# Optimization experiments

Hardware: AMD Instinct MI355X
Metric: run time of the kernel (lower is better)

The kernel has to match this reference:

```python
import jax, jax.numpy as jnp
import numpy as np

COST_CLASS, COST_BBOX, COST_MASK = 1.0, 5.0, 2.0
EPS = 1e-6


def setup_inputs() -> dict:
    key = jax.random.key(0)
    k = jax.random.split(key, 8)
    B, Q, M, C1, H, W = 8, 300, 100, 81, 128, 128
    pred_logits = jax.random.normal(k[0], (B, Q, C1), jnp.float32)
    # boxes as valid xyxy in [0,1]: lo in [0,.5], size in [0,.5]
    plo = jax.random.uniform(k[1], (B, Q, 2)) * 0.5
    psz = jax.random.uniform(k[2], (B, Q, 2)) * 0.5
    pred_boxes = jnp.concatenate([plo, plo + psz], axis=-1)
    pred_masks = jax.random.normal(k[3], (B, Q, H, W), jnp.float32)
    gt_labels = jax.random.randint(k[4], (B, M), 0, C1, dtype=jnp.int32)
    glo = jax.random.uniform(k[5], (B, M, 2)) * 0.5
    gsz = jax.random.uniform(k[6], (B, M, 2)) * 0.5
    gt_boxes = jnp.concatenate([glo, glo + gsz], axis=-1)
    gt_masks = (jax.random.uniform(k[7], (B, M, H, W)) > 0.5).astype(jnp.float32)
    valid = jnp.ones((B, M), jnp.bool_)
    return dict(pred_logits=pred_logits, pred_boxes=pred_boxes, pred_masks=pred_masks,
                gt_labels=gt_labels, gt_boxes=gt_boxes, gt_masks=gt_masks, valid=valid)


def _giou(b1, b2):
    # b1 [Q,4], b2 [M,4] (xyxy) -> [Q,M] generalized IoU
    lt = jnp.maximum(b1[:, None, :2], b2[None, :, :2])
    rb = jnp.minimum(b1[:, None, 2:], b2[None, :, 2:])
    wh = jnp.clip(rb - lt, 0.0)
    inter = wh[..., 0] * wh[..., 1]
    a1 = (b1[:, 2] - b1[:, 0]) * (b1[:, 3] - b1[:, 1])
    a2 = (b2[:, 2] - b2[:, 0]) * (b2[:, 3] - b2[:, 1])
    union = a1[:, None] + a2[None, :] - inter
    iou = inter / (union + EPS)
    ltm = jnp.minimum(b1[:, None, :2], b2[None, :, :2])
    rbm = jnp.maximum(b1[:, None, 2:], b2[None, :, 2:])
    whm = jnp.clip(rbm - ltm, 0.0)
    am = whm[..., 0] * whm[..., 1]
    return iou - (am - union) / (am + EPS)


@jax.jit
def _cost_matrix(pred_logits, pred_boxes, pred_masks, gt_labels, gt_boxes, gt_masks):
    B, Q = pred_logits.shape[:2]
    M = gt_labels.shape[1]
    probs = jax.nn.softmax(pred_logits, axis=-1)                      # [B,Q,C+1]
    idx = jnp.broadcast_to(gt_labels[:, None, :].astype(jnp.int32), (B, Q, M))
    cost_class = -jnp.take_along_axis(probs, idx, axis=2)             # [B,Q,M]
    # L1 cdist
    cost_bbox = jnp.abs(pred_boxes[:, :, None, :] - gt_boxes[:, None, :, :]).sum(-1)
    cost_giou = -jax.vmap(_giou)(pred_boxes, gt_boxes)                # [B,Q,M]
    # dice cost
    pm = jax.nn.sigmoid(pred_masks).reshape(B, Q, -1)                 # [B,Q,HW]
    gm = gt_masks.reshape(B, M, -1).astype(pm.dtype)                  # [B,M,HW]
    num = 2.0 * jnp.einsum('bqc,bmc->bqm', pm, gm)
    den = pm.sum(-1)[:, :, None] + gm.sum(-1)[:, None, :]
    cost_mask = 1.0 - num / (den + EPS)
    # NOTE: faithful to source quirk -- giou term is folded into cost_bbox
    # and therefore weighted by COST_BBOX.
    return (COST_CLASS * cost_class + COST_BBOX * (cost_bbox + cost_giou)
            + COST_MASK * cost_mask)


def _hungarian(cost):
    # Jonker-Volgenant style shortest-augmenting-path assignment (e-maxx).
    # cost: np [n,m] with n <= m. Returns p[m]: row assigned to each col (-1 if none).
    n, m = cost.shape
    u = np.zeros(n)
    v = np.zeros(m)
    p = np.full(m, -1, np.int64)
    for i in range(n):
        minv = np.full(m, np.inf)
        way = np.full(m, -1, np.int64)
        used = np.zeros(m, bool)
        cur_row, j0 = i, -1
        while True:
            cur = cost[cur_row] - u[cur_row] - v
            upd = (~used) & (cur < minv)
            minv[upd] = cur[upd]
            way[upd] = j0
            mv = np.where(used, np.inf, minv)
            j1 = int(np.argmin(mv))
            delta = mv[j1]
            u[i] += delta
            uj = np.nonzero(used)[0]
            if uj.size:
                u[p[uj]] += delta
                v[uj] -= delta
            minv[~used] -= delta
            used[j1] = True
            j0 = j1
            cur_row = p[j1]
            if cur_row == -1:
                break
        j = j0
        while j != -1:
            jp = way[j]
            p[j] = p[jp] if jp != -1 else i
            j = jp
    return p


def reference(pred_logits, pred_boxes, pred_masks, gt_labels, gt_boxes, gt_masks, valid):
    # valid is all-ones (num_gt == max_objects for every sample), so the
    # per-sample variable-size slicing in the torch loop reduces to full M.
    C = _cost_matrix(pred_logits, pred_boxes, pred_masks, gt_labels, gt_boxes, gt_masks)
    Cn = np.asarray(C, dtype=np.float64)
    preds, gts = [], []
    for b in range(Cn.shape[0]):
        # solve on transpose: rows = gt (M=100) <= cols = queries (Q=300)
        p = _hungarian(Cn[b].T)            # p[q] = matched gt index or -1
        q = np.nonzero(p >= 0)[0]          # sorted pred indices (scipy convention)
        preds.append(q)
        gts.append(p[q])
    pred_idx = jnp.asarray(np.stack(preds), dtype=jnp.int32)  # [B, M]
    gt_idx = jnp.asarray(np.stack(gts), dtype=jnp.int32)      # [B, M]
    return C, pred_idx, gt_idx
```

## Files before the change

kernel.cpp:

```cpp
#include <hip/hip_runtime.h>

#define HW 16384
#define NQ 300
#define NM 100
#define NB 8
#define NC 81
#define KCH 1024
#define NKC 16
#define CTP 304

typedef __attribute__((ext_vector_type(8))) short frag8;
typedef __attribute__((ext_vector_type(4))) float float4v;
typedef __attribute__((ext_vector_type(4))) unsigned short ushort4v;

__device__ __forceinline__ unsigned short f2bf(float f) {
  union { float f; unsigned u; } c; c.f = f;
  unsigned r = c.u + 0x7FFFu + ((c.u >> 16) & 1u);
  return (unsigned short)(r >> 16);
}

__global__ __launch_bounds__(256) void prep_kernel(
    const float* __restrict__ pmask, const float* __restrict__ gmask,
    unsigned short* __restrict__ pm, unsigned short* __restrict__ gm,
    float* __restrict__ psum, float* __restrict__ gsum) {
  int row = blockIdx.x;
  int t = threadIdx.x;
  bool isP = row < NB * NQ;
  const float* srcf = isP ? (pmask + (size_t)row * HW)
                          : (gmask + (size_t)(row - NB * NQ) * HW);
  unsigned short* dst = isP ? (pm + (size_t)row * HW)
                            : (gm + (size_t)(row - NB * NQ) * HW);
  const float4v* src = (const float4v*)srcf;
  float s = 0.f;
  for (int i = t; i < HW / 4; i += 256) {
    float4v x = src[i];
    float y0, y1, y2, y3;
    if (isP) {
      y0 = 1.f / (1.f + __expf(-x.x));
      y1 = 1.f / (1.f + __expf(-x.y));
      y2 = 1.f / (1.f + __expf(-x.z));
      y3 = 1.f / (1.f + __expf(-x.w));
    } else { y0 = x.x; y1 = x.y; y2 = x.z; y3 = x.w; }
    s += (y0 + y1) + (y2 + y3);
    ushort4v o = { f2bf(y0), f2bf(y1), f2bf(y2), f2bf(y3) };
    *(ushort4v*)(dst + i * 4) = o;
  }
  for (int off = 32; off > 0; off >>= 1) s += __shfl_xor(s, off, 64);
  __shared__ float red[4];
  int wave = t >> 6, lane = t & 63;
  if (lane == 0) red[wave] = s;
  __syncthreads();
  if (t == 0) {
    float tot = (red[0] + red[1]) + (red[2] + red[3]);
    if (isP) psum[row] = tot; else gsum[row - NB * NQ] = tot;
  }
}

__global__ __launch_bounds__(256) void softmax_kernel(
    const float* __restrict__ logits, float* __restrict__ probs) {
  int wave = threadIdx.x >> 6, lane = threadIdx.x & 63;
  int row = blockIdx.x * 4 + wave;
  const float* in = logits + (size_t)row * NC;
  float x0 = (lane < NC) ? in[lane] : -1e30f;
  float x1 = (lane + 64 < NC) ? in[lane + 64] : -1e30f;
  float mx = fmaxf(x0, x1);
  for (int off = 32; off > 0; off >>= 1) mx = fmaxf(mx, __shfl_xor(mx, off, 64));
  float e0 = (lane < NC) ? __expf(x0 - mx) : 0.f;
  float e1 = (lane + 64 < NC) ? __expf(x1 - mx) : 0.f;
  float s = e0 + e1;
  for (int off = 32; off > 0; off >>= 1) s += __shfl_xor(s, off, 64);
  float inv = 1.f / s;
  if (lane < NC) probs[(size_t)row * NC + lane] = e0 * inv;
  if (lane + 64 < NC) probs[(size_t)row * NC + lane + 64] = e1 * inv;
}

__global__ __launch_bounds__(64) void dot_kernel(
    const unsigned short* __restrict__ pm, const unsigned short* __restrict__ gm,
    float* __restrict__ dotv) {
  int qt = blockIdx.x;
  int b = blockIdx.y >> 4, kc = blockIdx.y & 15;
  int lane = threadIdx.x;
  int q0 = qt * 16;
  int row_a = q0 + (lane & 15);
  int ra = (row_a < NQ) ? row_a : NQ - 1;
  int koff = (lane >> 4) * 8;
  const unsigned short* pA = pm + ((size_t)b * NQ + ra) * HW + kc * KCH + koff;
  const unsigned short* pB0 = gm + (size_t)b * NM * HW + kc * KCH + koff;
  const unsigned short* pB[7];
#pragma unroll
  for (int mt = 0; mt < 7; ++mt) {
    int row_b = mt * 16 + (lane & 15);
    int rb = (row_b < NM) ? row_b : NM - 1;
    pB[mt] = pB0 + (size_t)rb * HW;
  }
  float4v acc[7];
#pragma unroll
  for (int mt = 0; mt < 7; ++mt) acc[mt] = (float4v){0.f, 0.f, 0.f, 0.f};
#pragma unroll 2
  for (int k = 0; k < KCH; k += 32) {
    frag8 a = *(const frag8*)(pA + k);
#pragma unroll
    for (int mt = 0; mt < 7; ++mt) {
      frag8 bb = *(const frag8*)(pB[mt] + k);
      acc[mt] = __builtin_amdgcn_mfma_f32_16x16x32_bf16(a, bb, acc[mt], 0, 0, 0);
    }
  }
#pragma unroll
  for (int mt = 0; mt < 7; ++mt) {
    int cm = mt * 16 + (lane & 15);
    if (cm < NM) {
#pragma unroll
      for (int r = 0; r < 4; ++r) {
        int cq = q0 + (lane >> 4) * 4 + r;
        if (cq < NQ)
          unsafeAtomicAdd(&dotv[((size_t)b * NQ + cq) * NM + cm], acc[mt][r]);
      }
    }
  }
}

__global__ __launch_bounds__(256) void combine_kernel(
    const float* __restrict__ dotv, const float* __restrict__ psum,
    const float* __restrict__ gsum, const float* __restrict__ probs,
    const int* __restrict__ labels, const float* __restrict__ pboxes,
    const float* __restrict__ gboxes, float* __restrict__ outC,
    float* __restrict__ ct) {
  int idx = blockIdx.x * 256 + threadIdx.x;
  if (idx >= NB * NQ * NM) return;
  int b = idx / (NQ * NM);
  int r = idx - b * (NQ * NM);
  int q = r / NM;
  int m = r - q * NM;
  float num = 2.f * dotv[idx];
  float den = psum[b * NQ + q] + gsum[b * NM + m];
  float cmask = 1.f - num / (den + 1e-6f);
  int lab = labels[b * NM + m];
  float cclass = -probs[((size_t)b * NQ + q) * NC + lab];
  const float* pb = pboxes + ((size_t)b * NQ + q) * 4;
  const float* gb = gboxes + ((size_t)b * NM + m) * 4;
  float p0 = pb[0], p1 = pb[1], p2 = pb[2], p3 = pb[3];
  float g0 = gb[0], g1 = gb[1], g2 = gb[2], g3 = gb[3];
  float cbbox = fabsf(p0 - g0) + fabsf(p1 - g1) + fabsf(p2 - g2) + fabsf(p3 - g3);
  float iw = fmaxf(fminf(p2, g2) - fmaxf(p0, g0), 0.f);
  float ih = fmaxf(fminf(p3, g3) - fmaxf(p1, g1), 0.f);
  float inter = iw * ih;
  float a1 = (p2 - p0) * (p3 - p1), a2 = (g2 - g0) * (g3 - g1);
  float uni = a1 + a2 - inter;
  float iou = inter / (uni + 1e-6f);
  float aw = fmaxf(fmaxf(p2, g2) - fminf(p0, g0), 0.f);
  float ah = fmaxf(fmaxf(p3, g3) - fminf(p1, g1), 0.f);
  float am = aw * ah;
  float giou = iou - (am - uni) / (am + 1e-6f);
  float C = cclass + 5.f * (cbbox - giou) + 2.f * cmask;
  outC[idx] = C;
  ct[((size_t)b * NM + m) * CTP + q] = C;
}

__device__ __forceinline__ float wave_fmin_bcast(float x) {
  int t;
  t = __builtin_amdgcn_update_dpp(__float_as_int(x), __float_as_int(x), 0x111, 0xf, 0xf, false);
  x = fminf(x, __int_as_float(t));
  t = __builtin_amdgcn_update_dpp(__float_as_int(x), __float_as_int(x), 0x112, 0xf, 0xf, false);
  x = fminf(x, __int_as_float(t));
  t = __builtin_amdgcn_update_dpp(__float_as_int(x), __float_as_int(x), 0x114, 0xf, 0xf, false);
  x = fminf(x, __int_as_float(t));
  t = __builtin_amdgcn_update_dpp(__float_as_int(x), __float_as_int(x), 0x118, 0xf, 0xf, false);
  x = fminf(x, __int_as_float(t));
  t = __builtin_amdgcn_update_dpp(__float_as_int(x), __float_as_int(x), 0x142, 0xf, 0xf, false);
  x = fminf(x, __int_as_float(t));
  t = __builtin_amdgcn_update_dpp(__float_as_int(x), __float_as_int(x), 0x143, 0xf, 0xf, false);
  x = fminf(x, __int_as_float(t));
  return __int_as_float(__builtin_amdgcn_readlane(__float_as_int(x), 63));
}

extern __shared__ char hsmem[];
__global__ __launch_bounds__(64) void hungarian_kernel(
    const float* __restrict__ ct, float* __restrict__ out) {
  float* cost   = (float*)hsmem;
  float* u      = (float*)(hsmem + 121600);
  int*   p      = (int*)(hsmem + 122000);
  int*   way    = (int*)(hsmem + 123280);
  int*   colOwn = (int*)(hsmem + 124560);
  int*   rowUsed= (int*)(hsmem + 125840);
  int*   queue  = (int*)(hsmem + 126240);
  int*   qmisc  = (int*)(hsmem + 127840);
  int*   flist  = colOwn;
  const int b = blockIdx.x;
  const int lane = threadIdx.x;
  const float INF = __builtin_inff();

  {
    const float4v* a4 = (const float4v*)(ct + (size_t)b * NM * CTP);
    float4v* c4 = (float4v*)cost;
    for (int i = lane; i < NM * CTP / 4; i += 64) c4[i] = a4[i];
  }
#pragma unroll
  for (int w = 0; w < 5; ++w) {
    p[lane + 64 * w] = -1;
    colOwn[lane + 64 * w] = 0x7fffffff;
  }
  if (lane == 0) { qmisc[0] = 0; qmisc[1] = 0; }
  float v[5];
#pragma unroll
  for (int w = 0; w < 5; ++w) v[w] = 0.f;
  __syncthreads();

  int rarg0 = 0, rarg1 = 0;
  {
    int i = lane;
    float mv = INF; int cj = 0;
    for (int j = 0; j < NQ; ++j) {
      float c = cost[i * CTP + j];
      if (c < mv) { mv = c; cj = j; }
    }
    u[i] = mv; rarg0 = cj;
  }
  if (lane < NM - 64) {
    int i = lane + 64;
    float mv = INF; int cj = 0;
    for (int j = 0; j < NQ; ++j) {
      float c = cost[i * CTP + j];
      if (c < mv) { mv = c; cj = j; }
    }
    u[i] = mv; rarg1 = cj;
  }
  atomicMin(&colOwn[rarg0], lane);
  if (lane < NM - 64) atomicMin(&colOwn[rarg1], lane + 64);
  __syncthreads();
  int free0 = 0, free1 = 0;
  {
    bool won = (colOwn[rarg0] == lane);
    if (won) p[rarg0] = lane;
    rowUsed[lane] = won ? 1 : 0;
    free0 = won ? 0 : 1;
  }
  if (lane < NM - 64) {
    bool won = (colOwn[rarg1] == lane + 64);
    if (won) p[rarg1] = lane + 64;
    rowUsed[lane + 64] = won ? 1 : 0;
    free1 = won ? 0 : 1;
  }
  {
    unsigned long long m0 = __ballot(free0 != 0);
    if (free0) queue[__popcll(m0 & ((1ull << lane) - 1ull))] = lane;
    int base = (int)__popcll(m0);
    unsigned long long m1 = __ballot(free1 != 0);
    if (free1) queue[base + (int)__popcll(m1 & ((1ull << lane) - 1ull))] = lane + 64;
    base += (int)__popcll(m1);
    if (lane == 0) qmisc[1] = base;
  }

  int pops = 0;
  while (true) {
    __syncthreads();
    int h = qmisc[0], t = qmisc[1];
    if (h >= t || pops >= 192) break;
    int i = queue[h];
    ++pops;
    if (lane == 0) qmisc[0] = h + 1;
    float tv[5];
    float m1 = INF, m2 = INF;
#pragma unroll
    for (int w = 0; w < 5; ++w) {
      int j = lane + 64 * w;
      float tt = (j < NQ) ? (cost[i * CTP + j] - v[w]) : INF;
      tv[w] = tt;
      if (tt < m1) { m2 = m1; m1 = tt; } else if (tt < m2) m2 = tt;
    }
    float m1g = wave_fmin_bcast(m1);
    int j1 = -1;
#pragma unroll
    for (int w = 0; w < 5; ++w) {
      unsigned long long mk = __ballot(tv[w] == m1g);
      if (j1 < 0 && mk) j1 = (int)__builtin_ctzll(mk) + 64 * w;
    }
    float c2c = INF;
#pragma unroll
    for (int w = 0; w < 5; ++w)
      if (lane + 64 * w != j1) c2c = fminf(c2c, tv[w]);
    float c2 = wave_fmin_bcast(c2c);
    float delta = (c2 > m1g) ? (c2 - m1g) : 0.f;
    int i1 = p[j1];
    if (i1 >= 0 && delta <= 0.f) {
      if (lane == 0) u[i] = c2;
      continue;
    }
#pragma unroll
    for (int w = 0; w < 5; ++w) if (lane + 64 * w == j1) v[w] -= delta;
    if (lane == 0) {
      u[i] = c2;
      p[j1] = i;
      rowUsed[i] = 1;
      if (i1 >= 0) { rowUsed[i1] = 0; queue[t] = i1; qmisc[1] = t + 1; }
    }
  }
  __syncthreads();

  int nfree;
  {
    int r0 = rowUsed[lane];
    int r1 = (lane < NM - 64) ? rowUsed[lane + 64] : 1;
    unsigned long long m0 = __ballot(r0 == 0);
    if (!r0) flist[__popcll(m0 & ((1ull << lane) - 1ull))] = lane;
    int base = (int)__popcll(m0);
    unsigned long long m1 = __ballot(r1 == 0);
    if (!r1) flist[base + (int)__popcll(m1 & ((1ull << lane) - 1ull))] = lane + 64;
    nfree = base + (int)__popcll(m1);
  }
  __syncthreads();

  int pr0, pr1, pr2, pr3, pr4;
  float ur0, ur1;
  pr0 = p[lane]; pr1 = p[lane + 64]; pr2 = p[lane + 128];
  pr3 = p[lane + 192]; pr4 = p[lane + 256];
  ur0 = u[lane];
  ur1 = (lane < NM - 64) ? u[lane + 64] : 0.f;

  for (int fi = 0; fi < nfree; ++fi) {
    int i = flist[fi];
    float dv[5]; int usedR[5];
#pragma unroll
    for (int w = 0; w < 5; ++w) {
      int j = lane + 64 * w;
      dv[w] = INF;
      usedR[w] = (j >= NQ) ? 1 : 0;
      way[j] = -1;
    }
    float S = 0.f;
    int nr = i, j0 = -1;
    while (true) {
      float urow;
      {
        int bits = (nr < 64)
            ? __builtin_amdgcn_readlane(__float_as_int(ur0), nr & 63)
            : __builtin_amdgcn_readlane(__float_as_int(ur1), nr & 63);
        urow = __int_as_float(bits);
      }
      int base = nr * CTP;
      float c0 = cost[base + lane];
      float c1 = cost[base + lane + 64];
      float c2_ = cost[base + lane + 128];
      float c3 = cost[base + lane + 192];
      float c4 = cost[base + lane + 256];
      float cr[5] = {c0, c1, c2_, c3, c4};
      float cmin = INF;
#pragma unroll
      for (int w = 0; w < 5; ++w) {
        if (!usedR[w]) {
          float cand = S + cr[w] - urow - v[w];
          if (cand < dv[w]) { dv[w] = cand; way[lane + 64 * w] = j0; }
          cmin = fminf(cmin, dv[w]);
        }
      }
      float m = wave_fmin_bcast(cmin);
      int j1 = -1;
#pragma unroll
      for (int w = 0; w < 5; ++w) {
        unsigned long long mk = __ballot(!usedR[w] && dv[w] == m);
        if (j1 < 0 && mk) j1 = (int)__builtin_ctzll(mk) + 64 * w;
      }
      S = m;
#pragma unroll
      for (int w = 0; w < 5; ++w) if (lane + 64 * w == j1) usedR[w] = 1;
      j0 = j1;
      int nr2;
      {
        int sl = j1 >> 6, ln = j1 & 63;
        if (sl == 0)      nr2 = __builtin_amdgcn_readlane(pr0, ln);
        else if (sl == 1) nr2 = __builtin_amdgcn_readlane(pr1, ln);
        else if (sl == 2) nr2 = __builtin_amdgcn_readlane(pr2, ln);
        else if (sl == 3) nr2 = __builtin_amdgcn_readlane(pr3, ln);
        else              nr2 = __builtin_amdgcn_readlane(pr4, ln);
      }
      if (nr2 < 0) break;
      nr = nr2;
    }
#pragma unroll
    for (int w = 0; w < 5; ++w) {
      int j = lane + 64 * w;
      if (j < NQ && usedR[w]) {
        float amt = S - dv[w];
        v[w] -= amt;
        int pj = (w == 0) ? pr0 : (w == 1) ? pr1 : (w == 2) ? pr2
               : (w == 3) ? pr3 : pr4;
        if (pj >= 0) u[pj] += amt;
      }
    }
    if (lane == 0) u[i] += S;
    __syncthreads();
    if (lane == 0) {
      int j = j0;
      while (j != -1) {
        int jp = way[j];
        p[j] = (jp != -1) ? p[jp] : i;
        j = jp;
      }
    }
    __syncthreads();
    pr0 = p[lane]; pr1 = p[lane + 64]; pr2 = p[lane + 128];
    pr3 = p[lane + 192]; pr4 = p[lane + 256];
    ur0 = u[lane];
    ur1 = (lane < NM - 64) ? u[lane + 64] : 0.f;
  }

  {
    float* po = out + NB * NQ * NM + b * NM;
    float* go = out + NB * NQ * NM + NB * NM + b * NM;
    int base = 0;
#pragma unroll
    for (int w = 0; w < 5; ++w) {
      int j = lane + 64 * w;
      int pj = (j < NQ) ? p[j] : -1;
      unsigned long long mask = __ballot(pj >= 0);
      if (pj >= 0) {
        int pos = base + (int)__popcll(mask & ((1ull << lane) - 1ull));
        po[pos] = (float)j;
        go[pos] = (float)pj;
      }
      base += (int)__popcll(mask);
    }
  }
}

extern "C" void kernel_launch(void* const* d_in, const int* in_sizes, int n_in,
                              void* d_out, int out_size, void* d_ws, size_t ws_size,
                              hipStream_t stream) {
  const float* logits = (const float*)d_in[0];
  const float* pboxes = (const float*)d_in[1];
  const float* pmask  = (const float*)d_in[2];
  const int*   labels = (const int*)d_in[3];
  const float* gboxes = (const float*)d_in[4];
  const float* gmask  = (const float*)d_in[5];
  float* out = (float*)d_out;
  char* ws = (char*)d_ws;

  unsigned short* pm   = (unsigned short*)(ws + 0);
  unsigned short* gmb  = (unsigned short*)(ws + 78643200);
  float* psum  = (float*)(ws + 104857600);
  float* gsum  = (float*)(ws + 104867200);
  float* probs = (float*)(ws + 104870400);
  float* dotv  = (float*)(ws + 105648000);
  float* ct    = (float*)(ws + 106608000);

  hipFuncSetAttribute(reinterpret_cast<const void*>(hungarian_kernel),
                      hipFuncAttributeMaxDynamicSharedMemorySize, 127872);

  hipMemsetAsync(dotv, 0, NB * NQ * NM * sizeof(float), stream);
  hipLaunchKernelGGL(prep_kernel, dim3(NB * NQ + NB * NM), dim3(256), 0, stream,
                     pmask, gmask, pm, gmb, psum, gsum);
  hipLaunchKernelGGL(softmax_kernel, dim3(600), dim3(256), 0, stream, logits, probs);
  hipLaunchKernelGGL(dot_kernel, dim3(19, NB * NKC), dim3(64), 0, stream, pm, gmb, dotv);
  hipLaunchKernelGGL(combine_kernel, dim3((NB * NQ * NM + 255) / 256), dim3(256), 0, stream,
                     dotv, psum, gsum, probs, labels, pboxes, gboxes, out, ct);
  hipLaunchKernelGGL(hungarian_kernel, dim3(NB), dim3(64), 127872, stream, ct, out);
}
```

Measured before the change: 494.7 us.

## Keep auction queue and assignment in registers, fuse min/second-min reductions, prefetch rows

The auction phase of the single-wave Hungarian kernel moves its queue, column-owner array and row-used flags out of shared memory. They now live in per-lane registers and wave ballot masks, which removes the per-iteration __syncthreads and the LDS round trips. The min and second-min reductions are merged into one DPP pass, and the next queued row's costs are prefetched before the reduction. The initial row-argmin scan staggers each lane's starting column to avoid LDS bank conflicts, with an explicit lowest-index tie-break. This adds register pressure and more complex lane-select logic.

```diff
diff --git a/kernel.cpp b/kernel.cpp
--- a/kernel.cpp
+++ b/kernel.cpp
@@ -173,6 +173,23 @@
   return __int_as_float(__builtin_amdgcn_readlane(__float_as_int(x), 63));
 }
 
+#define PAIR_STEP(PAT)                                                         \
+  {                                                                            \
+    int t1 = __builtin_amdgcn_update_dpp(__float_as_int(m1), __float_as_int(m1), PAT, 0xf, 0xf, false); \
+    int t2 = __builtin_amdgcn_update_dpp(__float_as_int(m2), __float_as_int(m2), PAT, 0xf, 0xf, false); \
+    float o1 = __int_as_float(t1), o2 = __int_as_float(t2);                    \
+    float hi = fmaxf(m1, o1);                                                  \
+    m1 = fminf(m1, o1);                                                        \
+    m2 = fminf(fminf(m2, o2), hi);                                             \
+  }
+__device__ __forceinline__ void wave_fmin2_bcast(float m1, float m2,
+                                                 float* g1, float* g2) {
+  PAIR_STEP(0x111) PAIR_STEP(0x112) PAIR_STEP(0x114) PAIR_STEP(0x118)
+  PAIR_STEP(0x142) PAIR_STEP(0x143)
+  *g1 = __int_as_float(__builtin_amdgcn_readlane(__float_as_int(m1), 63));
+  *g2 = __int_as_float(__builtin_amdgcn_readlane(__float_as_int(m2), 63));
+}
+
 extern __shared__ char hsmem[];
 __global__ __launch_bounds__(64) void hungarian_kernel(
     const float* __restrict__ ct, float* __restrict__ out) {
@@ -181,9 +198,7 @@
   int*   p      = (int*)(hsmem + 122000);
   int*   way    = (int*)(hsmem + 123280);
   int*   colOwn = (int*)(hsmem + 124560);
-  int*   rowUsed= (int*)(hsmem + 125840);
-  int*   queue  = (int*)(hsmem + 126240);
-  int*   qmisc  = (int*)(hsmem + 127840);
+  int*   queue  = (int*)(hsmem + 125840);
   int*   flist  = colOwn;
   const int b = blockIdx.x;
   const int lane = threadIdx.x;
@@ -199,7 +214,6 @@
     p[lane + 64 * w] = -1;
     colOwn[lane + 64 * w] = 0x7fffffff;
   }
-  if (lane == 0) { qmisc[0] = 0; qmisc[1] = 0; }
   float v[5];
 #pragma unroll
   for (int w = 0; w < 5; ++w) v[w] = 0.f;
@@ -207,114 +221,156 @@
 
   int rarg0 = 0, rarg1 = 0;
   {
-    int i = lane;
-    float mv = INF; int cj = 0;
-    for (int j = 0; j < NQ; ++j) {
-      float c = cost[i * CTP + j];
-      if (c < mv) { mv = c; cj = j; }
-    }
-    u[i] = mv; rarg0 = cj;
-  }
-  if (lane < NM - 64) {
-    int i = lane + 64;
-    float mv = INF; int cj = 0;
-    for (int j = 0; j < NQ; ++j) {
-      float c = cost[i * CTP + j];
-      if (c < mv) { mv = c; cj = j; }
-    }
-    u[i] = mv; rarg1 = cj;
+    int o = (17 * lane) & 31;
+    float mv0 = INF, mv1 = INF;
+    int cj0 = 0x7fffffff, cj1 = 0x7fffffff;
+    bool two = lane < NM - 64;
+    for (int t = 0; t < CTP; ++t) {
+      int jj = t + o; if (jj >= CTP) jj -= CTP;
+      float c0 = cost[lane * CTP + jj];
+      float c1 = two ? cost[(lane + 64) * CTP + jj] : 0.f;
+      if (jj < NQ) {
+        if (c0 < mv0 || (c0 == mv0 && jj < cj0)) { mv0 = c0; cj0 = jj; }
+        if (two && (c1 < mv1 || (c1 == mv1 && jj < cj1))) { mv1 = c1; cj1 = jj; }
+      }
+    }
+    u[lane] = mv0; rarg0 = cj0;
+    if (two) { u[lane + 64] = mv1; rarg1 = cj1; }
   }
   atomicMin(&colOwn[rarg0], lane);
   if (lane < NM - 64) atomicMin(&colOwn[rarg1], lane + 64);
   __syncthreads();
-  int free0 = 0, free1 = 0;
-  {
-    bool won = (colOwn[rarg0] == lane);
-    if (won) p[rarg0] = lane;
-    rowUsed[lane] = won ? 1 : 0;
-    free0 = won ? 0 : 1;
-  }
-  if (lane < NM - 64) {
-    bool won = (colOwn[rarg1] == lane + 64);
-    if (won) p[rarg1] = lane + 64;
-    rowUsed[lane + 64] = won ? 1 : 0;
-    free1 = won ? 0 : 1;
-  }
+  unsigned long long ru0, ru1;
+  int free0, free1;
+  {
+    bool won0 = (colOwn[rarg0] == lane);
+    if (won0) p[rarg0] = lane;
+    free0 = won0 ? 0 : 1;
+    bool won1 = (lane < NM - 64) && (colOwn[rarg1] == lane + 64);
+    if (won1) p[rarg1] = lane + 64;
+    free1 = ((lane < NM - 64) && !won1) ? 1 : 0;
+    ru0 = __ballot(won0);
+    ru1 = __ballot(won1);
+  }
+  int qt_;
   {
     unsigned long long m0 = __ballot(free0 != 0);
     if (free0) queue[__popcll(m0 & ((1ull << lane) - 1ull))] = lane;
     int base = (int)__popcll(m0);
     unsigned long long m1 = __ballot(free1 != 0);
     if (free1) queue[base + (int)__popcll(m1 & ((1ull << lane) - 1ull))] = lane + 64;
-    base += (int)__popcll(m1);
-    if (lane == 0) qmisc[1] = base;
-  }
-
-  int pops = 0;
-  while (true) {
-    __syncthreads();
-    int h = qmisc[0], t = qmisc[1];
-    if (h >= t || pops >= 192) break;
-    int i = queue[h];
-    ++pops;
-    if (lane == 0) qmisc[0] = h + 1;
-    float tv[5];
-    float m1 = INF, m2 = INF;
-#pragma unroll
-    for (int w = 0; w < 5; ++w) {
-      int j = lane + 64 * w;
-      float tt = (j < NQ) ? (cost[i * CTP + j] - v[w]) : INF;
-      tv[w] = tt;
-      if (tt < m1) { m2 = m1; m1 = tt; } else if (tt < m2) m2 = tt;
-    }
-    float m1g = wave_fmin_bcast(m1);
-    int j1 = -1;
-#pragma unroll
-    for (int w = 0; w < 5; ++w) {
-      unsigned long long mk = __ballot(tv[w] == m1g);
-      if (j1 < 0 && mk) j1 = (int)__builtin_ctzll(mk) + 64 * w;
-    }
-    float c2c = INF;
-#pragma unroll
-    for (int w = 0; w < 5; ++w)
-      if (lane + 64 * w != j1) c2c = fminf(c2c, tv[w]);
-    float c2 = wave_fmin_bcast(c2c);
-    float delta = (c2 > m1g) ? (c2 - m1g) : 0.f;
-    int i1 = p[j1];
-    if (i1 >= 0 && delta <= 0.f) {
+    qt_ = base + (int)__popcll(m1);
+  }
+  __syncthreads();
+  int q0 = queue[lane], q1 = queue[lane + 64], q2 = queue[lane + 128],
+      q3 = queue[lane + 192], q4 = queue[lane + 256];
+  int pr0 = p[lane], pr1 = p[lane + 64], pr2 = p[lane + 128],
+      pr3 = p[lane + 192], pr4 = p[lane + 256];
+
+#define QREAD(pos, dst)                                                  \
+  { int _w = (pos) >> 6, _l = (pos) & 63;                                \
+    if (_w == 0)      dst = __builtin_amdgcn_readlane(q0, _l);           \
+    else if (_w == 1) dst = __builtin_amdgcn_readlane(q1, _l);           \
+    else if (_w == 2) dst = __builtin_amdgcn_readlane(q2, _l);           \
+    else if (_w == 3) dst = __builtin_amdgcn_readlane(q3, _l);           \
+    else              dst = __builtin_amdgcn_readlane(q4, _l); }
+#define QWRITE(pos, val)                                                 \
+  { int _w = (pos) >> 6, _l = (pos) & 63;                                \
+    if (_w == 0)      { if (lane == _l) q0 = (val); }                    \
+    else if (_w == 1) { if (lane == _l) q1 = (val); }                    \
+    else if (_w == 2) { if (lane == _l) q2 = (val); }                    \
+    else if (_w == 3) { if (lane == _l) q3 = (val); }                    \
+    else              { if (lane == _l) q4 = (val); } }
+#define PREAD(pos, dst)                                                  \
+  { int _w = (pos) >> 6, _l = (pos) & 63;                                \
+    if (_w == 0)      dst = __builtin_amdgcn_readlane(pr0, _l);          \
+    else if (_w == 1) dst = __builtin_amdgcn_readlane(pr1, _l);          \
+    else if (_w == 2) dst = __builtin_amdgcn_readlane(pr2, _l);          \
+    else if (_w == 3) dst = __builtin_amdgcn_readlane(pr3, _l);          \
+    else              dst = __builtin_amdgcn_readlane(pr4, _l); }
+#define PWRITE(pos, val)                                                 \
+  { int _w = (pos) >> 6, _l = (pos) & 63;                                \
+    if (_w == 0)      { if (lane == _l) pr0 = (val); }                   \
+    else if (_w == 1) { if (lane == _l) pr1 = (val); }                   \
+    else if (_w == 2) { if (lane == _l) pr2 = (val); }                   \
+    else if (_w == 3) { if (lane == _l) pr3 = (val); }                   \
+    else              { if (lane == _l) pr4 = (val); } }
+
+  float pf0 = 0.f, pf1 = 0.f, pf2 = 0.f, pf3 = 0.f, pf4 = 0.f;
+  int pfrow = -1;
+  int j4c = lane + 256; if (j4c > 303) j4c = 303;
+#define PFETCH(r)                                                        \
+  { int _base = (r) * CTP;                                               \
+    pf0 = cost[_base + lane];        pf1 = cost[_base + lane + 64];      \
+    pf2 = cost[_base + lane + 128];  pf3 = cost[_base + lane + 192];     \
+    pf4 = cost[_base + j4c];         pfrow = (r); }
+
+  {
+    int h = 0, tl = qt_, pops = 0;
+    int nexti = -1;
+    if (h < tl) { QREAD(h, nexti); PFETCH(nexti); }
+    while (nexti >= 0 && pops < 192) {
+      int i = nexti; ++h; ++pops;
+      if (pfrow != i) PFETCH(i);
+      float t0 = pf0 - v[0];
+      float t1 = pf1 - v[1];
+      float t2 = pf2 - v[2];
+      float t3 = pf3 - v[3];
+      float t4 = (lane + 256 < NQ) ? (pf4 - v[4]) : INF;
+      float m1 = INF, m2 = INF;
+#define INS(x) { if ((x) < m1) { m2 = m1; m1 = (x); } else if ((x) < m2) m2 = (x); }
+      INS(t0) INS(t1) INS(t2) INS(t3) INS(t4)
+#undef INS
+      nexti = -1;
+      if (h < tl) { QREAD(h, nexti); PFETCH(nexti); }
+      float m1g, c2;
+      wave_fmin2_bcast(m1, m2, &m1g, &c2);
+      int j1 = -1;
+      {
+        unsigned long long mk;
+        mk = __ballot(t0 == m1g); if (mk) j1 = (int)__builtin_ctzll(mk);
+        if (j1 < 0) { mk = __ballot(t1 == m1g); if (mk) j1 = (int)__builtin_ctzll(mk) + 64; }
+        if (j1 < 0) { mk = __ballot(t2 == m1g); if (mk) j1 = (int)__builtin_ctzll(mk) + 128; }
+        if (j1 < 0) { mk = __ballot(t3 == m1g); if (mk) j1 = (int)__builtin_ctzll(mk) + 192; }
+        if (j1 < 0) { mk = __ballot(t4 == m1g); if (mk) j1 = (int)__builtin_ctzll(mk) + 256; }
+      }
+      float delta = (c2 > m1g) ? (c2 - m1g) : 0.f;
+      int i1; PREAD(j1, i1);
+      if (i1 >= 0 && delta <= 0.f) {
+        if (lane == 0) u[i] = c2;
+        continue;
+      }
+#pragma unroll
+      for (int w = 0; w < 5; ++w) if (lane + 64 * w == j1) v[w] -= delta;
       if (lane == 0) u[i] = c2;
-      continue;
-    }
-#pragma unroll
-    for (int w = 0; w < 5; ++w) if (lane + 64 * w == j1) v[w] -= delta;
-    if (lane == 0) {
-      u[i] = c2;
-      p[j1] = i;
-      rowUsed[i] = 1;
-      if (i1 >= 0) { rowUsed[i1] = 0; queue[t] = i1; qmisc[1] = t + 1; }
-    }
-  }
+      PWRITE(j1, i);
+      if (i < 64) ru0 |= 1ull << i; else ru1 |= 1ull << (i - 64);
+      if (i1 >= 0) {
+        if (i1 < 64) ru0 &= ~(1ull << i1); else ru1 &= ~(1ull << (i1 - 64));
+        QWRITE(tl, i1); ++tl;
+        if (nexti < 0) { nexti = i1; PFETCH(i1); }
+      }
+    }
+  }
+  p[lane] = pr0; p[lane + 64] = pr1; p[lane + 128] = pr2;
+  p[lane + 192] = pr3; p[lane + 256] = pr4;
   __syncthreads();
 
   int nfree;
   {
-    int r0 = rowUsed[lane];
-    int r1 = (lane < NM - 64) ? rowUsed[lane + 64] : 1;
-    unsigned long long m0 = __ballot(r0 == 0);
-    if (!r0) flist[__popcll(m0 & ((1ull << lane) - 1ull))] = lane;
-    int base = (int)__popcll(m0);
-    unsigned long long m1 = __ballot(r1 == 0);
-    if (!r1) flist[base + (int)__popcll(m1 & ((1ull << lane) - 1ull))] = lane + 64;
-    nfree = base + (int)__popcll(m1);
+    unsigned long long f0 = ~ru0;
+    unsigned long long f1 = (~ru1) & ((1ull << (NM - 64)) - 1ull);
+    int r0 = (int)((f0 >> lane) & 1ull);
+    int r1 = (lane < NM - 64) ? (int)((f1 >> lane) & 1ull) : 0;
+    if (r0) flist[__popcll(f0 & ((1ull << lane) - 1ull))] = lane;
+    int base = (int)__popcll(f0);
+    if (r1) flist[base + (int)__popcll(f1 & ((1ull << lane) - 1ull))] = lane + 64;
+    nfree = base + (int)__popcll(f1);
   }
   __syncthreads();
 
-  int pr0, pr1, pr2, pr3, pr4;
-  float ur0, ur1;
-  pr0 = p[lane]; pr1 = p[lane + 64]; pr2 = p[lane + 128];
-  pr3 = p[lane + 192]; pr4 = p[lane + 256];
-  ur0 = u[lane];
-  ur1 = (lane < NM - 64) ? u[lane + 64] : 0.f;
+  float ur0 = u[lane];
+  float ur1 = (lane < NM - 64) ? u[lane + 64] : 0.f;
 
   for (int fi = 0; fi < nfree; ++fi) {
     int i = flist[fi];
@@ -363,15 +419,7 @@
 #pragma unroll
       for (int w = 0; w < 5; ++w) if (lane + 64 * w == j1) usedR[w] = 1;
       j0 = j1;
-      int nr2;
-      {
-        int sl = j1 >> 6, ln = j1 & 63;
-        if (sl == 0)      nr2 = __builtin_amdgcn_readlane(pr0, ln);
-        else if (sl == 1) nr2 = __builtin_amdgcn_readlane(pr1, ln);
-        else if (sl == 2) nr2 = __builtin_amdgcn_readlane(pr2, ln);
-        else if (sl == 3) nr2 = __builtin_amdgcn_readlane(pr3, ln);
-        else              nr2 = __builtin_amdgcn_readlane(pr4, ln);
-      }
+      int nr2; PREAD(j1, nr2);
       if (nr2 < 0) break;
       nr = nr2;
     }
@@ -407,10 +455,11 @@
     float* po = out + NB * NQ * NM + b * NM;
     float* go = out + NB * NQ * NM + NB * NM + b * NM;
     int base = 0;
+    int prw[5] = {pr0, pr1, pr2, pr3, pr4};
 #pragma unroll
     for (int w = 0; w < 5; ++w) {
       int j = lane + 64 * w;
-      int pj = (j < NQ) ? p[j] : -1;
+      int pj = (j < NQ) ? prw[w] : -1;
       unsigned long long mask = __ballot(pj >= 0);
       if (pj >= 0) {
         int pos = base + (int)__popcll(mask & ((1ull << lane) - 1ull));
@@ -443,7 +492,7 @@
   float* ct    = (float*)(ws + 106608000);
 
   hipFuncSetAttribute(reinterpret_cast<const void*>(hungarian_kernel),
-                      hipFuncAttributeMaxDynamicSharedMemorySize, 127872);
+                      hipFuncAttributeMaxDynamicSharedMemorySize, 127168);
 
   hipMemsetAsync(dotv, 0, NB * NQ * NM * sizeof(float), stream);
   hipLaunchKernelGGL(prep_kernel, dim3(NB * NQ + NB * NM), dim3(256), 0, stream,
@@ -452,5 +501,5 @@
   hipLaunchKernelGGL(dot_kernel, dim3(19, NB * NKC), dim3(64), 0, stream, pm, gmb, dotv);
   hipLaunchKernelGGL(combine_kernel, dim3((NB * NQ * NM + 255) / 256), dim3(256), 0, stream,
                      dotv, psum, gsum, probs, labels, pboxes, gboxes, out, ct);
-  hipLaunchKernelGGL(hungarian_kernel, dim3(NB), dim3(64), 127872, stream, ct, out);
-}
+  hipLaunchKernelGGL(hungarian_kernel, dim3(NB), dim3(64), 127168, stream, ct, out);
+}
```

After: 547.9 us. 1.11x slower.

## Fuse pred-mask sigmoid and bf16 conversion into the MFMA dot kernel

Applied to the files above, without the earlier changes.

The separate prep pass over predicted masks is removed. The dot kernel now reads the fp32 mask logits directly, applies the sigmoid, packs the results to bf16 fragments on the fly, and adds the per-row sigmoid sums into psum with atomics. This avoids writing and re-reading a large intermediate bf16 buffer, at the cost of more ALU work and fp32 loads inside the MFMA loop. The Hungarian kernel also moves rowUsed into static shared memory and takes the final assignment from registers, which are minor tweaks.

```diff
diff --git a/kernel.cpp b/kernel.cpp
--- a/kernel.cpp
+++ b/kernel.cpp
@@ -19,30 +19,18 @@
   return (unsigned short)(r >> 16);
 }
 
-__global__ __launch_bounds__(256) void prep_kernel(
-    const float* __restrict__ pmask, const float* __restrict__ gmask,
-    unsigned short* __restrict__ pm, unsigned short* __restrict__ gm,
-    float* __restrict__ psum, float* __restrict__ gsum) {
+__global__ __launch_bounds__(256) void gmprep_kernel(
+    const float* __restrict__ gmask, unsigned short* __restrict__ gm,
+    float* __restrict__ gsum) {
   int row = blockIdx.x;
   int t = threadIdx.x;
-  bool isP = row < NB * NQ;
-  const float* srcf = isP ? (pmask + (size_t)row * HW)
-                          : (gmask + (size_t)(row - NB * NQ) * HW);
-  unsigned short* dst = isP ? (pm + (size_t)row * HW)
-                            : (gm + (size_t)(row - NB * NQ) * HW);
-  const float4v* src = (const float4v*)srcf;
+  const float4v* src = (const float4v*)(gmask + (size_t)row * HW);
+  unsigned short* dst = gm + (size_t)row * HW;
   float s = 0.f;
   for (int i = t; i < HW / 4; i += 256) {
     float4v x = src[i];
-    float y0, y1, y2, y3;
-    if (isP) {
-      y0 = 1.f / (1.f + __expf(-x.x));
-      y1 = 1.f / (1.f + __expf(-x.y));
-      y2 = 1.f / (1.f + __expf(-x.z));
-      y3 = 1.f / (1.f + __expf(-x.w));
-    } else { y0 = x.x; y1 = x.y; y2 = x.z; y3 = x.w; }
-    s += (y0 + y1) + (y2 + y3);
-    ushort4v o = { f2bf(y0), f2bf(y1), f2bf(y2), f2bf(y3) };
+    s += (x.x + x.y) + (x.z + x.w);
+    ushort4v o = { f2bf(x.x), f2bf(x.y), f2bf(x.z), f2bf(x.w) };
     *(ushort4v*)(dst + i * 4) = o;
   }
   for (int off = 32; off > 0; off >>= 1) s += __shfl_xor(s, off, 64);
@@ -50,10 +38,7 @@
   int wave = t >> 6, lane = t & 63;
   if (lane == 0) red[wave] = s;
   __syncthreads();
-  if (t == 0) {
-    float tot = (red[0] + red[1]) + (red[2] + red[3]);
-    if (isP) psum[row] = tot; else gsum[row - NB * NQ] = tot;
-  }
+  if (t == 0) gsum[row] = (red[0] + red[1]) + (red[2] + red[3]);
 }
 
 __global__ __launch_bounds__(256) void softmax_kernel(
@@ -75,8 +60,8 @@
 }
 
 __global__ __launch_bounds__(64) void dot_kernel(
-    const unsigned short* __restrict__ pm, const unsigned short* __restrict__ gm,
-    float* __restrict__ dotv) {
+    const float* __restrict__ pmask, const unsigned short* __restrict__ gm,
+    float* __restrict__ dotv, float* __restrict__ psum) {
   int qt = blockIdx.x;
   int b = blockIdx.y >> 4, kc = blockIdx.y & 15;
   int lane = threadIdx.x;
@@ -84,7 +69,7 @@
   int row_a = q0 + (lane & 15);
   int ra = (row_a < NQ) ? row_a : NQ - 1;
   int koff = (lane >> 4) * 8;
-  const unsigned short* pA = pm + ((size_t)b * NQ + ra) * HW + kc * KCH + koff;
+  const float* pA = pmask + ((size_t)b * NQ + ra) * HW + kc * KCH + koff;
   const unsigned short* pB0 = gm + (size_t)b * NM * HW + kc * KCH + koff;
   const unsigned short* pB[7];
 #pragma unroll
@@ -96,15 +81,32 @@
   float4v acc[7];
 #pragma unroll
   for (int mt = 0; mt < 7; ++mt) acc[mt] = (float4v){0.f, 0.f, 0.f, 0.f};
+  float asum = 0.f;
 #pragma unroll 2
   for (int k = 0; k < KCH; k += 32) {
-    frag8 a = *(const frag8*)(pA + k);
+    float4v x0 = *(const float4v*)(pA + k);
+    float4v x1 = *(const float4v*)(pA + k + 4);
+    float s0 = 1.f / (1.f + __expf(-x0.x));
+    float s1 = 1.f / (1.f + __expf(-x0.y));
+    float s2 = 1.f / (1.f + __expf(-x0.z));
+    float s3 = 1.f / (1.f + __expf(-x0.w));
+    float s4 = 1.f / (1.f + __expf(-x1.x));
+    float s5 = 1.f / (1.f + __expf(-x1.y));
+    float s6 = 1.f / (1.f + __expf(-x1.z));
+    float s7 = 1.f / (1.f + __expf(-x1.w));
+    asum += ((s0 + s1) + (s2 + s3)) + ((s4 + s5) + (s6 + s7));
+    frag8 a;
+    a[0] = (short)f2bf(s0); a[1] = (short)f2bf(s1);
+    a[2] = (short)f2bf(s2); a[3] = (short)f2bf(s3);
+    a[4] = (short)f2bf(s4); a[5] = (short)f2bf(s5);
+    a[6] = (short)f2bf(s6); a[7] = (short)f2bf(s7);
 #pragma unroll
     for (int mt = 0; mt < 7; ++mt) {
       frag8 bb = *(const frag8*)(pB[mt] + k);
       acc[mt] = __builtin_amdgcn_mfma_f32_16x16x32_bf16(a, bb, acc[mt], 0, 0, 0);
     }
   }
+  if (row_a < NQ) unsafeAtomicAdd(&psum[b * NQ + row_a], asum);
 #pragma unroll
   for (int mt = 0; mt < 7; ++mt) {
     int cm = mt * 16 + (lane & 15);
@@ -181,9 +183,8 @@
   int*   p      = (int*)(hsmem + 122000);
   int*   way    = (int*)(hsmem + 123280);
   int*   colOwn = (int*)(hsmem + 124560);
-  int*   rowUsed= (int*)(hsmem + 125840);
-  int*   queue  = (int*)(hsmem + 126240);
-  int*   qmisc  = (int*)(hsmem + 127840);
+  int*   queue  = (int*)(hsmem + 125840);
+  int*   qmisc  = (int*)(hsmem + 127440);
   int*   flist  = colOwn;
   const int b = blockIdx.x;
   const int lane = threadIdx.x;
@@ -231,15 +232,21 @@
   {
     bool won = (colOwn[rarg0] == lane);
     if (won) p[rarg0] = lane;
-    rowUsed[lane] = won ? 1 : 0;
+    if (lane < NM) {}
     free0 = won ? 0 : 1;
   }
+  int rowUsed0 = free0 ? 0 : 1;
+  int rowUsed1 = 0;
   if (lane < NM - 64) {
     bool won = (colOwn[rarg1] == lane + 64);
     if (won) p[rarg1] = lane + 64;
-    rowUsed[lane + 64] = won ? 1 : 0;
+    rowUsed1 = won ? 1 : 0;
     free1 = won ? 0 : 1;
   }
+  __shared__ int rowUsedA[NM];
+  rowUsedA[lane < NM ? lane : 0] = 0;
+  rowUsedA[lane] = rowUsed0;
+  if (lane < NM - 64) rowUsedA[lane + 64] = rowUsed1;
   {
     unsigned long long m0 = __ballot(free0 != 0);
     if (free0) queue[__popcll(m0 & ((1ull << lane) - 1ull))] = lane;
@@ -290,16 +297,16 @@
     if (lane == 0) {
       u[i] = c2;
       p[j1] = i;
-      rowUsed[i] = 1;
-      if (i1 >= 0) { rowUsed[i1] = 0; queue[t] = i1; qmisc[1] = t + 1; }
+      rowUsedA[i] = 1;
+      if (i1 >= 0) { rowUsedA[i1] = 0; queue[t] = i1; qmisc[1] = t + 1; }
     }
   }
   __syncthreads();
 
   int nfree;
   {
-    int r0 = rowUsed[lane];
-    int r1 = (lane < NM - 64) ? rowUsed[lane + 64] : 1;
+    int r0 = rowUsedA[lane];
+    int r1 = (lane < NM - 64) ? rowUsedA[lane + 64] : 1;
     unsigned long long m0 = __ballot(r0 == 0);
     if (!r0) flist[__popcll(m0 & ((1ull << lane) - 1ull))] = lane;
     int base = (int)__popcll(m0);
@@ -407,10 +414,11 @@
     float* po = out + NB * NQ * NM + b * NM;
     float* go = out + NB * NQ * NM + NB * NM + b * NM;
     int base = 0;
+    int prw[5] = {pr0, pr1, pr2, pr3, pr4};
 #pragma unroll
     for (int w = 0; w < 5; ++w) {
       int j = lane + 64 * w;
-      int pj = (j < NQ) ? p[j] : -1;
+      int pj = (j < NQ) ? prw[w] : -1;
       unsigned long long mask = __ballot(pj >= 0);
       if (pj >= 0) {
         int pos = base + (int)__popcll(mask & ((1ull << lane) - 1ull));
@@ -434,23 +442,23 @@
   float* out = (float*)d_out;
   char* ws = (char*)d_ws;
 
-  unsigned short* pm   = (unsigned short*)(ws + 0);
-  unsigned short* gmb  = (unsigned short*)(ws + 78643200);
-  float* psum  = (float*)(ws + 104857600);
-  float* gsum  = (float*)(ws + 104867200);
-  float* probs = (float*)(ws + 104870400);
-  float* dotv  = (float*)(ws + 105648000);
-  float* ct    = (float*)(ws + 106608000);
+  unsigned short* gmb  = (unsigned short*)(ws + 0);
+  float* dotv  = (float*)(ws + 26214400);
+  float* psum  = (float*)(ws + 27174400);
+  float* gsum  = (float*)(ws + 27184000);
+  float* probs = (float*)(ws + 27187200);
+  float* ct    = (float*)(ws + 27964800);
 
   hipFuncSetAttribute(reinterpret_cast<const void*>(hungarian_kernel),
-                      hipFuncAttributeMaxDynamicSharedMemorySize, 127872);
-
-  hipMemsetAsync(dotv, 0, NB * NQ * NM * sizeof(float), stream);
-  hipLaunchKernelGGL(prep_kernel, dim3(NB * NQ + NB * NM), dim3(256), 0, stream,
-                     pmask, gmask, pm, gmb, psum, gsum);
+                      hipFuncAttributeMaxDynamicSharedMemorySize, 127472);
+
+  hipMemsetAsync(dotv, 0, NB * NQ * NM * sizeof(float) + NB * NQ * sizeof(float), stream);
+  hipLaunchKernelGGL(gmprep_kernel, dim3(NB * NM), dim3(256), 0, stream,
+                     gmask, gmb, gsum);
   hipLaunchKernelGGL(softmax_kernel, dim3(600), dim3(256), 0, stream, logits, probs);
-  hipLaunchKernelGGL(dot_kernel, dim3(19, NB * NKC), dim3(64), 0, stream, pm, gmb, dotv);
+  hipLaunchKernelGGL(dot_kernel, dim3(19, NB * NKC), dim3(64), 0, stream,
+                     pmask, gmb, dotv, psum);
   hipLaunchKernelGGL(combine_kernel, dim3((NB * NQ * NM + 255) / 256), dim3(256), 0, stream,
                      dotv, psum, gsum, probs, labels, pboxes, gboxes, out, ct);
-  hipLaunchKernelGGL(hungarian_kernel, dim3(NB), dim3(64), 127872, stream, ct, out);
-}
+  hipLaunchKernelGGL(hungarian_kernel, dim3(NB), dim3(64), 127472, stream, ct, out);
+}
```

New measurement: 471.1 us. 4.8% less time.
